# Performance work log

Hardware: AMD Instinct MI355X
Metric: run time of the kernel (lower is better)

Reference implementation:

```python
import jax, jax.numpy as jnp
import numpy as np

NUM_GROUPS = 32
EPS = 1e-6


def group_norm(x, w, b):
    # x: (B, C, L); normalize per group of C//32 channels over (channels-in-group, L)
    B, C, L = x.shape
    xg = x.reshape(B, NUM_GROUPS, C // NUM_GROUPS, L)
    mean = jnp.mean(xg, axis=(2, 3), keepdims=True)
    var = jnp.var(xg, axis=(2, 3), keepdims=True)
    xn = ((xg - mean) * jax.lax.rsqrt(var + EPS)).reshape(B, C, L)
    return xn * w[None, :, None] + b[None, :, None]


def conv1x1(x, w, b):
    # 1x1 Conv1d == channel-mixing linear. x: (B,C,L), w: (O,C), b: (O,)
    return jnp.einsum('oc,bcl->bol', w, x) + b[None, :, None]


def setup_inputs() -> dict:
    key = jax.random.key(0)
    ks = jax.random.split(key, 6)
    B, C, L = 8, 512, 2048
    s = 1.0 / np.sqrt(C)
    return {
        'x': jax.random.normal(ks[0], (B, C, L), dtype=jnp.float32),
        'gn_w': jnp.ones((C,), jnp.float32),
        'gn_b': jnp.zeros((C,), jnp.float32),
        'wq': jax.random.normal(ks[1], (C, C), dtype=jnp.float32) * s,
        'bq': jnp.zeros((C,), jnp.float32),
        'wk': jax.random.normal(ks[2], (C, C), dtype=jnp.float32) * s,
        'bk': jnp.zeros((C,), jnp.float32),
        'wv': jax.random.normal(ks[3], (C, C), dtype=jnp.float32) * s,
        'bv': jnp.zeros((C,), jnp.float32),
        'wo': jax.random.normal(ks[4], (C, C), dtype=jnp.float32) * s,
        'bo': jnp.zeros((C,), jnp.float32),
    }


def reference(x, gn_w, gn_b, wq, bq, wk, bk, wv, bv, wo, bo):
    B, C, L = x.shape
    h = group_norm(x, gn_w, gn_b)
    q = conv1x1(h, wq, bq)  # (B,C,L)
    k = conv1x1(h, wk, bk)
    v = conv1x1(h, wv, bv)
    scale = jnp.asarray(C, x.dtype) ** -0.5
    # scores over length: w[b,i,j] = sum_c q[b,c,i] k[b,c,j]
    w_ = jnp.einsum('bci,bcj->bij', q, k) * scale
    w_ = jax.nn.softmax(w_, axis=-1)
    # h[b,c,i] = sum_j w[b,i,j] v[b,c,j]
    h = jnp.einsum('bij,bcj->bci', w_, v)
    h = conv1x1(h, wo, bo)
    return x + h
```

## Files before the change

kernel.cpp:

```cpp
#include <hip/hip_runtime.h>
#include <math.h>

#define BATCH 8
#define CH 512
#define LEN 2048
#define NG 32
#define CPG 16

typedef unsigned short u16;
typedef __bf16 bf16x8 __attribute__((ext_vector_type(8)));
typedef float f32x16 __attribute__((ext_vector_type(16)));

__device__ __forceinline__ u16 f2bf(float f) {
    union { float f; unsigned u; } c; c.f = f;
    unsigned r = c.u + 0x7fffu + ((c.u >> 16) & 1u);
    return (u16)(r >> 16);
}
__device__ __forceinline__ float bf2f(u16 h) {
    union { unsigned u; float f; } c; c.u = ((unsigned)h) << 16;
    return c.f;
}
__device__ __forceinline__ void gload16(const u16* g, u16* l) {
    __builtin_amdgcn_global_load_lds(
        (const __attribute__((address_space(1))) unsigned int*)g,
        (__attribute__((address_space(3))) unsigned int*)l, 16, 0, 0);
}

__global__ __launch_bounds__(256) void fused_pre(
    const float* __restrict__ x,
    const float* __restrict__ w0, const float* __restrict__ w1,
    const float* __restrict__ w2, const float* __restrict__ w3,
    u16* __restrict__ o0, u16* __restrict__ o1,
    u16* __restrict__ o2, u16* __restrict__ o3,
    float4* __restrict__ zbuf, float* __restrict__ stats) {
    const int blk = blockIdx.x;
    if (blk < 16) {
        zbuf[blk * 256 + threadIdx.x] = make_float4(0.f, 0.f, 0.f, 0.f);
    } else if (blk < 1040) {
        const int wb = blk - 16;
        const float* s; u16* d;
        switch (wb >> 8) {
            case 0: s = w0; d = o0; break;
            case 1: s = w1; d = o1; break;
            case 2: s = w2; d = o2; break;
            default: s = w3; d = o3; break;
        }
        const int i = (wb & 255) * 256 + threadIdx.x;
        float4 f = ((const float4*)s)[i];
        ((ushort4*)d)[i] = make_ushort4(f2bf(f.x), f2bf(f.y), f2bf(f.z), f2bf(f.w));
    } else {
        const int sb = blk - 1040;
        const int b = sb >> 7, g = (sb >> 2) & 31, sl = sb & 3;
        const float4* xp = (const float4*)(x + ((size_t)b * CH + (size_t)g * CPG) * LEN) + sl * 2048;
        float s = 0.f, s2 = 0.f;
        #pragma unroll
        for (int i = 0; i < 8; ++i) {
            float4 v = xp[threadIdx.x + i * 256];
            s += v.x + v.y + v.z + v.w;
            s2 = fmaf(v.x, v.x, fmaf(v.y, v.y, fmaf(v.z, v.z, fmaf(v.w, v.w, s2))));
        }
        #pragma unroll
        for (int off = 32; off > 0; off >>= 1) {
            s  += __shfl_down(s, off, 64);
            s2 += __shfl_down(s2, off, 64);
        }
        __shared__ float sm[2][4];
        const int lane = threadIdx.x & 63, wv = threadIdx.x >> 6;
        if (lane == 0) { sm[0][wv] = s; sm[1][wv] = s2; }
        __syncthreads();
        if (threadIdx.x == 0) {
            const int base = (b * NG + g) * 4 + sl;
            stats[base]        = sm[0][0] + sm[0][1] + sm[0][2] + sm[0][3];
            stats[1024 + base] = sm[1][0] + sm[1][1] + sm[1][2] + sm[1][3];
        }
    }
}

__global__ __launch_bounds__(256) void gn_apply_t(const float* __restrict__ x,
                                                  const float* __restrict__ stats,
                                                  const float* __restrict__ gw,
                                                  const float* __restrict__ gb,
                                                  u16* __restrict__ Ht) {
    __shared__ float tile[64][65];
    const int b = blockIdx.z, c0 = blockIdx.y * 64, l0 = blockIdx.x * 64;
    const int t = threadIdx.x;
    const int rid = t >> 4, q = t & 15;
    const float inv = 1.f / (CPG * LEN);
    #pragma unroll
    for (int pass = 0; pass < 4; ++pass) {
        const int c = rid + pass * 16;
        const int ca = c0 + c;
        const int base = (b * NG + (ca >> 4)) * 4;
        const float S  = stats[base + 0] + stats[base + 1] + stats[base + 2] + stats[base + 3];
        const float S2 = stats[1024 + base + 0] + stats[1024 + base + 1]
                       + stats[1024 + base + 2] + stats[1024 + base + 3];
        const float mean = S * inv;
        const float var  = S2 * inv - mean * mean;
        const float a  = rsqrtf(var + 1e-6f) * gw[ca];
        const float sh = gb[ca] - mean * a;
        const float4 v = *(const float4*)&x[((size_t)b * CH + ca) * LEN + l0 + q * 4];
        tile[c][q * 4 + 0] = v.x * a + sh;
        tile[c][q * 4 + 1] = v.y * a + sh;
        tile[c][q * 4 + 2] = v.z * a + sh;
        tile[c][q * 4 + 3] = v.w * a + sh;
    }
    __syncthreads();
    #pragma unroll
    for (int pass = 0; pass < 4; ++pass) {
        const int l = rid + pass * 16;
        ushort4 o;
        o.x = f2bf(tile[q * 4 + 0][l]);
        o.y = f2bf(tile[q * 4 + 1][l]);
        o.z = f2bf(tile[q * 4 + 2][l]);
        o.w = f2bf(tile[q * 4 + 3][l]);
        *(ushort4*)&Ht[((size_t)b * LEN + l0 + l) * CH + c0 + q * 4] = o;
    }
}

#define EPI_QK   0
#define EPI_TNRM 3
#define EPI_FIN  4

template <int MODE>
__global__ __launch_bounds__(256, 4) void gemm_bt(
    const u16* __restrict__ A, int lda, long long sA,
    const u16* __restrict__ B, int ldb, long long sB,
    void* __restrict__ Out, void* __restrict__ Out2,
    int ldo, long long sO,
    const float* __restrict__ bias, const float* __restrict__ bias2,
    const float* __restrict__ res, long long sR,
    float* __restrict__ rsum, long long sRS,
    int K, float alpha) {
    __shared__ u16 As[128 * 64];
    __shared__ u16 Bs[128 * 64];

    int bz, by, bx;
    if (MODE == EPI_TNRM) {
        const int gx = gridDim.x, gy = gridDim.y;
        int flat = (blockIdx.z * gy + blockIdx.y) * gx + blockIdx.x;
        const int nbk = gx * gy * (int)gridDim.z;
        flat = (flat & 7) * (nbk >> 3) + (flat >> 3);
        bz = flat / (gx * gy);
        const int rr = flat - bz * gx * gy;
        by = rr & 3;
        bx = rr >> 2;
    } else {
        bz = blockIdx.z; by = blockIdx.y; bx = blockIdx.x;
    }
    const int n0 = bx * 128, m0 = by * 128;
    A += (size_t)bz * sA;
    B += (size_t)bz * sB;
    const int t = threadIdx.x;
    const int lane = t & 63, wid = t >> 6;

    const int rowL = t >> 3, kq = (t & 7) ^ (rowL & 7);
    unsigned aoff = (unsigned)((m0 + rowL) * lda + kq * 8);
    unsigned boff = (unsigned)((n0 + rowL) * ldb + kq * 8);
    u16* const lds_dst_a = As + t * 8;
    u16* const lds_dst_b = Bs + t * 8;

    f32x16 acc[2][2];
    #pragma unroll
    for (int i = 0; i < 2; ++i)
        #pragma unroll
        for (int j = 0; j < 2; ++j)
            acc[i][j] = (f32x16)(0.f);

    const int col = lane & 31, half = lane >> 5;
    const int wm = (wid & 1) * 64, wn = (wid >> 1) * 64;
    const int mf = wm + col, nf = wn + col;
    const int mswz = mf & 7, nswz = nf & 7;

    for (int k0 = 0; k0 < K; k0 += 64) {
        #pragma unroll
        for (int g = 0; g < 4; ++g) {
            gload16(A + aoff + g * (32 * lda), lds_dst_a + g * 2048);
            gload16(B + boff + g * (32 * ldb), lds_dst_b + g * 2048);
        }
        aoff += 64; boff += 64;
        __syncthreads();
        #pragma unroll
        for (int ks = 0; ks < 4; ++ks) {
            const int kcA = ((ks * 2 + half) ^ mswz) * 8;
            const int kcB = ((ks * 2 + half) ^ nswz) * 8;
            bf16x8 a0 = *(const bf16x8*)(As + (mf)      * 64 + kcA);
            bf16x8 a1 = *(const bf16x8*)(As + (mf + 32) * 64 + kcA);
            bf16x8 b0 = *(const bf16x8*)(Bs + (nf)      * 64 + kcB);
            bf16x8 b1 = *(const bf16x8*)(Bs + (nf + 32) * 64 + kcB);
            acc[0][0] = __builtin_amdgcn_mfma_f32_32x32x16_bf16(a0, b0, acc[0][0], 0, 0, 0);
            acc[0][1] = __builtin_amdgcn_mfma_f32_32x32x16_bf16(a0, b1, acc[0][1], 0, 0, 0);
            acc[1][0] = __builtin_amdgcn_mfma_f32_32x32x16_bf16(a1, b0, acc[1][0], 0, 0, 0);
            acc[1][1] = __builtin_amdgcn_mfma_f32_32x32x16_bf16(a1, b1, acc[1][1], 0, 0, 0);
        }
        __syncthreads();
    }

    if (MODE == EPI_FIN) {
        float* O = (float*)Out + (size_t)bz * sO;
        const float* R = res + (size_t)bz * sR;
        #pragma unroll
        for (int im = 0; im < 2; ++im)
            #pragma unroll
            for (int g4 = 0; g4 < 4; ++g4) {
                const int mb = m0 + wm + im * 32 + g4 * 8 + half * 4;
                #pragma unroll
                for (int jn = 0; jn < 2; ++jn) {
                    const int n = n0 + wn + jn * 32 + col;
                    const float bb = bias[n];
                    const size_t base = (size_t)n * ldo + mb;
                    const float4 r4 = *(const float4*)&R[base];
                    float4 o4;
                    o4.x = acc[im][jn][g4 * 4 + 0] + bb + r4.x;
                    o4.y = acc[im][jn][g4 * 4 + 1] + bb + r4.y;
                    o4.z = acc[im][jn][g4 * 4 + 2] + bb + r4.z;
                    o4.w = acc[im][jn][g4 * 4 + 3] + bb + r4.w;
                    *(float4*)&O[base] = o4;
                }
            }
    } else {
        u16* O;
        const float* bi = bias;
        const float* RS = (MODE == EPI_TNRM) ? rsum + (size_t)bz * sRS : nullptr;
        int mbase = m0 + wm;
        if (MODE == EPI_QK) {
            const bool hi = (m0 & 512) != 0;
            O  = (u16*)(hi ? Out2 : Out) + (size_t)bz * sO;
            bi = hi ? bias2 : bias;
            mbase = (m0 & 511) + wm;
        } else {
            O = (u16*)Out + (size_t)bz * sO;
        }
        float inv[2];
        if (MODE == EPI_TNRM) {
            inv[0] = 1.f / RS[n0 + wn + col];
            inv[1] = 1.f / RS[n0 + wn + 32 + col];
        }
        #pragma unroll
        for (int im = 0; im < 2; ++im)
            #pragma unroll
            for (int g4 = 0; g4 < 4; ++g4) {
                const int mb = mbase + im * 32 + g4 * 8 + half * 4;
                float4 bm = make_float4(0.f, 0.f, 0.f, 0.f);
                if (MODE == EPI_QK) bm = *(const float4*)&bi[mb];
                #pragma unroll
                for (int jn = 0; jn < 2; ++jn) {
                    const int n = n0 + wn + jn * 32 + col;
                    float v0 = acc[im][jn][g4 * 4 + 0];
                    float v1 = acc[im][jn][g4 * 4 + 1];
                    float v2 = acc[im][jn][g4 * 4 + 2];
                    float v3 = acc[im][jn][g4 * 4 + 3];
                    if (MODE == EPI_QK)  { v0 += bm.x; v1 += bm.y; v2 += bm.z; v3 += bm.w; }
                    if (MODE == EPI_TNRM) { v0 *= inv[jn]; v1 *= inv[jn]; v2 *= inv[jn]; v3 *= inv[jn]; }
                    ushort4 pk = make_ushort4(f2bf(v0), f2bf(v1), f2bf(v2), f2bf(v3));
                    *(ushort4*)&O[(size_t)n * ldo + mb] = pk;
                }
            }
    }
}

__global__ __launch_bounds__(256, 4) void gemm_sv(
    const u16* __restrict__ Kt, const u16* __restrict__ Qt,
    const u16* __restrict__ Ht, const u16* __restrict__ Wvb,
    u16* __restrict__ Sb, u16* __restrict__ Vb,
    const float* __restrict__ bv, float* __restrict__ rowsum,
    float alpha) {
    __shared__ u16 As[128 * 64];
    __shared__ u16 Bs[128 * 64];

    const long long sH = (long long)LEN * CH;
    const int blk = blockIdx.x;
    const bool isV = blk >= 2048;
    int bz, by, bx;
    const u16 *A, *B;
    u16* O;
    if (!isV) {
        int flat = (blk & 7) * 256 + (blk >> 3);
        bz = flat >> 8;
        const int rr = flat & 255;
        by = rr >> 4; bx = rr & 15;
        A = Kt + (size_t)bz * sH;
        B = Qt + (size_t)bz * sH;
        O = Sb + (size_t)bz * ((long long)LEN * LEN);
    } else {
        const int v = blk - 2048;
        bz = v >> 6;
        const int rr = v & 63;
        by = rr >> 2; bx = rr & 3;
        A = Ht + (size_t)bz * sH;
        B = Wvb;
        O = Vb + (size_t)bz * ((long long)CH * LEN);
    }

    const int n0 = bx * 128, m0 = by * 128;
    const int t = threadIdx.x;
    const int lane = t & 63, wid = t >> 6;

    const int rowL = t >> 3, kq = (t & 7) ^ (rowL & 7);
    unsigned aoff = (unsigned)((m0 + rowL) * CH + kq * 8);
    unsigned boff = (unsigned)((n0 + rowL) * CH + kq * 8);
    u16* const lds_dst_a = As + t * 8;
    u16* const lds_dst_b = Bs + t * 8;

    f32x16 acc[2][2];
    #pragma unroll
    for (int i = 0; i < 2; ++i)
        #pragma unroll
        for (int j = 0; j < 2; ++j)
            acc[i][j] = (f32x16)(0.f);

    const int col = lane & 31, half = lane >> 5;
    const int wm = (wid & 1) * 64, wn = (wid >> 1) * 64;
    const int mf = wm + col, nf = wn + col;
    const int mswz = mf & 7, nswz = nf & 7;

    for (int k0 = 0; k0 < CH; k0 += 64) {
        #pragma unroll
        for (int g = 0; g < 4; ++g) {
            gload16(A + aoff + g * (32 * CH), lds_dst_a + g * 2048);
            gload16(B + boff + g * (32 * CH), lds_dst_b + g * 2048);
        }
        aoff += 64; boff += 64;
        __syncthreads();
        #pragma unroll
        for (int ks = 0; ks < 4; ++ks) {
            const int kcA = ((ks * 2 + half) ^ mswz) * 8;
            const int kcB = ((ks * 2 + half) ^ nswz) * 8;
            bf16x8 a0 = *(const bf16x8*)(As + (mf)      * 64 + kcA);
            bf16x8 a1 = *(const bf16x8*)(As + (mf + 32) * 64 + kcA);
            bf16x8 b0 = *(const bf16x8*)(Bs + (nf)      * 64 + kcB);
            bf16x8 b1 = *(const bf16x8*)(Bs + (nf + 32) * 64 + kcB);
            acc[0][0] = __builtin_amdgcn_mfma_f32_32x32x16_bf16(a0, b0, acc[0][0], 0, 0, 0);
            acc[0][1] = __builtin_amdgcn_mfma_f32_32x32x16_bf16(a0, b1, acc[0][1], 0, 0, 0);
            acc[1][0] = __builtin_amdgcn_mfma_f32_32x32x16_bf16(a1, b0, acc[1][0], 0, 0, 0);
            acc[1][1] = __builtin_amdgcn_mfma_f32_32x32x16_bf16(a1, b1, acc[1][1], 0, 0, 0);
        }
        __syncthreads();
    }

    if (!isV) {
        float* RS = rowsum + (size_t)bz * LEN;
        float psum[2] = {0.f, 0.f};
        #pragma unroll
        for (int im = 0; im < 2; ++im)
            #pragma unroll
            for (int g4 = 0; g4 < 4; ++g4) {
                const int mb = m0 + wm + im * 32 + g4 * 8 + half * 4;
                #pragma unroll
                for (int jn = 0; jn < 2; ++jn) {
                    const int n = n0 + wn + jn * 32 + col;
                    u16 h0 = f2bf(__expf(acc[im][jn][g4 * 4 + 0] * alpha));
                    u16 h1 = f2bf(__expf(acc[im][jn][g4 * 4 + 1] * alpha));
                    u16 h2 = f2bf(__expf(acc[im][jn][g4 * 4 + 2] * alpha));
                    u16 h3 = f2bf(__expf(acc[im][jn][g4 * 4 + 3] * alpha));
                    psum[jn] += bf2f(h0) + bf2f(h1) + bf2f(h2) + bf2f(h3);
                    *(ushort4*)&O[(size_t)n * LEN + mb] = make_ushort4(h0, h1, h2, h3);
                }
            }
        #pragma unroll
        for (int jn = 0; jn < 2; ++jn) psum[jn] += __shfl_xor(psum[jn], 32, 64);
        if (half == 0) {
            #pragma unroll
            for (int jn = 0; jn < 2; ++jn)
                atomicAdd(&RS[n0 + wn + jn * 32 + col], psum[jn]);
        }
    } else {
        #pragma unroll
        for (int im = 0; im < 2; ++im)
            #pragma unroll
            for (int g4 = 0; g4 < 4; ++g4) {
                const int mb = m0 + wm + im * 32 + g4 * 8 + half * 4;
                #pragma unroll
                for (int jn = 0; jn < 2; ++jn) {
                    const int n = n0 + wn + jn * 32 + col;
                    const float bb = bv[n];
                    ushort4 pk = make_ushort4(f2bf(acc[im][jn][g4 * 4 + 0] + bb),
                                              f2bf(acc[im][jn][g4 * 4 + 1] + bb),
                                              f2bf(acc[im][jn][g4 * 4 + 2] + bb),
                                              f2bf(acc[im][jn][g4 * 4 + 3] + bb));
                    *(ushort4*)&O[(size_t)n * LEN + mb] = pk;
                }
            }
    }
}

extern "C" void kernel_launch(void* const* d_in, const int* in_sizes, int n_in,
                              void* d_out, int out_size, void* d_ws, size_t ws_size,
                              hipStream_t stream) {
    const float* x    = (const float*)d_in[0];
    const float* gn_w = (const float*)d_in[1];
    const float* gn_b = (const float*)d_in[2];
    const float* wq   = (const float*)d_in[3];
    const float* bq   = (const float*)d_in[4];
    const float* wk   = (const float*)d_in[5];
    const float* bk   = (const float*)d_in[6];
    const float* wv   = (const float*)d_in[7];
    const float* bv   = (const float*)d_in[8];
    const float* wo   = (const float*)d_in[9];
    const float* bo   = (const float*)d_in[10];
    float* out = (float*)d_out;

    char* p = (char*)d_ws;
    const size_t WSZ = (size_t)CH * CH * 2;
    const size_t HSZ = (size_t)BATCH * CH * LEN * 2;
    u16* Wqk = (u16*)p; p += 2 * WSZ;
    u16* Wvb = (u16*)p; p += WSZ;
    u16* Wob = (u16*)p; p += WSZ;
    u16* Ht  = (u16*)p; p += HSZ;
    u16* Qt  = (u16*)p; p += HSZ;
    u16* Kt  = (u16*)p; p += HSZ;
    u16* Vb  = (u16*)p; p += HSZ;
    u16* Sb  = (u16*)p; p += (size_t)BATCH * LEN * LEN * 2;
    float* rowsum = (float*)p; p += (size_t)BATCH * LEN * 4;
    float* stats  = (float*)p;

    const long long sH = (long long)LEN * CH;
    const long long sV = (long long)CH * LEN;
    const float scale = 0.04419417382415922f;

    fused_pre<<<2064, 256, 0, stream>>>(x, wq, wk, wv, wo,
                                        Wqk, Wqk + (size_t)CH * CH, Wvb, Wob,
                                        (float4*)rowsum, stats);
    gn_apply_t<<<dim3(LEN / 64, CH / 64, BATCH), 256, 0, stream>>>(x, stats, gn_w, gn_b, Ht);

    gemm_bt<EPI_QK><<<dim3(16, 8, 8), 256, 0, stream>>>(
        Wqk, CH, 0, Ht, CH, sH, Qt, Kt, CH, sH, bq, bk, nullptr, 0, nullptr, 0, CH, 0.f);
    gemm_sv<<<2560, 256, 0, stream>>>(Kt, Qt, Ht, Wvb, Sb, Vb, bv, rowsum, scale);
    gemm_bt<EPI_TNRM><<<dim3(16, 4, 8), 256, 0, stream>>>(
        Vb, LEN, sV, Sb, LEN, (long long)LEN * LEN, Ht, nullptr, CH, sH,
        nullptr, nullptr, nullptr, 0, rowsum, LEN, LEN, 0.f);
    gemm_bt<EPI_FIN><<<dim3(4, 16, 8), 256, 0, stream>>>(
        Ht, CH, sH, Wob, CH, 0, out, nullptr, LEN, sV, bo, nullptr, x, sV, nullptr, 0, CH, 0.f);
}
```

Baseline: 264.5 us.

## Fold output projection into value weights and fuse PV with final epilogue

Precomputes Wo·Wv in fp32 inside the prep kernel, along with a combined bias Wo·bv+bo, so the value GEMM produces Wo·V directly. The separate output-projection GEMM is removed. The P·V GEMM now writes the final fp32 output with rowsum normalization, bias and residual applied in its epilogue. This drops one 512-K GEMM and one bf16 intermediate round trip, at the cost of a slow scalar fp32 512x512x512 product in a 64-block prep section and different rounding.

```diff
diff --git a/kernel.cpp b/kernel.cpp
--- a/kernel.cpp
+++ b/kernel.cpp
@@ -28,34 +28,67 @@
 
 __global__ __launch_bounds__(256) void fused_pre(
     const float* __restrict__ x,
-    const float* __restrict__ w0, const float* __restrict__ w1,
-    const float* __restrict__ w2, const float* __restrict__ w3,
-    u16* __restrict__ o0, u16* __restrict__ o1,
-    u16* __restrict__ o2, u16* __restrict__ o3,
+    const float* __restrict__ wq, const float* __restrict__ wk,
+    const float* __restrict__ wv, const float* __restrict__ wo,
+    const float* __restrict__ bv, const float* __restrict__ bo,
+    u16* __restrict__ oq, u16* __restrict__ ok,
+    u16* __restrict__ wov, float* __restrict__ biasp,
     float4* __restrict__ zbuf, float* __restrict__ stats) {
     const int blk = blockIdx.x;
+    const int t = threadIdx.x;
     if (blk < 16) {
-        zbuf[blk * 256 + threadIdx.x] = make_float4(0.f, 0.f, 0.f, 0.f);
-    } else if (blk < 1040) {
+        zbuf[blk * 256 + t] = make_float4(0.f, 0.f, 0.f, 0.f);
+    } else if (blk < 528) {
         const int wb = blk - 16;
-        const float* s; u16* d;
-        switch (wb >> 8) {
-            case 0: s = w0; d = o0; break;
-            case 1: s = w1; d = o1; break;
-            case 2: s = w2; d = o2; break;
-            default: s = w3; d = o3; break;
-        }
-        const int i = (wb & 255) * 256 + threadIdx.x;
+        const float* s = (wb >> 8) ? wk : wq;
+        u16* d = (wb >> 8) ? ok : oq;
+        const int i = (wb & 255) * 256 + t;
         float4 f = ((const float4*)s)[i];
         ((ushort4*)d)[i] = make_ushort4(f2bf(f.x), f2bf(f.y), f2bf(f.z), f2bf(f.w));
+    } else if (blk < 592) {
+        const int b = blk - 528;
+        const int o0 = (b >> 3) * 64, c0 = (b & 7) * 64;
+        const int o = o0 + (t >> 4) * 4, c = c0 + (t & 15) * 4;
+        float acc[4][4] = {};
+        for (int k0 = 0; k0 < 512; k0 += 4) {
+            float4 A4[4], B4[4];
+            #pragma unroll
+            for (int r = 0; r < 4; ++r) A4[r] = *(const float4*)&wo[(size_t)(o + r) * 512 + k0];
+            #pragma unroll
+            for (int kk = 0; kk < 4; ++kk) B4[kk] = *(const float4*)&wv[(size_t)(k0 + kk) * 512 + c];
+            #pragma unroll
+            for (int r = 0; r < 4; ++r) {
+                const float ar[4] = {A4[r].x, A4[r].y, A4[r].z, A4[r].w};
+                #pragma unroll
+                for (int kk = 0; kk < 4; ++kk) {
+                    acc[r][0] = fmaf(ar[kk], B4[kk].x, acc[r][0]);
+                    acc[r][1] = fmaf(ar[kk], B4[kk].y, acc[r][1]);
+                    acc[r][2] = fmaf(ar[kk], B4[kk].z, acc[r][2]);
+                    acc[r][3] = fmaf(ar[kk], B4[kk].w, acc[r][3]);
+                }
+            }
+        }
+        #pragma unroll
+        for (int r = 0; r < 4; ++r)
+            *(ushort4*)&wov[(size_t)(o + r) * 512 + c] =
+                make_ushort4(f2bf(acc[r][0]), f2bf(acc[r][1]), f2bf(acc[r][2]), f2bf(acc[r][3]));
+    } else if (blk < 594) {
+        const int o = (blk - 592) * 256 + t;
+        float s = 0.f;
+        for (int kk = 0; kk < 512; kk += 4) {
+            float4 w4 = *(const float4*)&wo[(size_t)o * 512 + kk];
+            float4 b4 = *(const float4*)&bv[kk];
+            s = fmaf(w4.x, b4.x, fmaf(w4.y, b4.y, fmaf(w4.z, b4.z, fmaf(w4.w, b4.w, s))));
+        }
+        biasp[o] = s + bo[o];
     } else {
-        const int sb = blk - 1040;
+        const int sb = blk - 594;
         const int b = sb >> 7, g = (sb >> 2) & 31, sl = sb & 3;
         const float4* xp = (const float4*)(x + ((size_t)b * CH + (size_t)g * CPG) * LEN) + sl * 2048;
         float s = 0.f, s2 = 0.f;
         #pragma unroll
         for (int i = 0; i < 8; ++i) {
-            float4 v = xp[threadIdx.x + i * 256];
+            float4 v = xp[t + i * 256];
             s += v.x + v.y + v.z + v.w;
             s2 = fmaf(v.x, v.x, fmaf(v.y, v.y, fmaf(v.z, v.z, fmaf(v.w, v.w, s2))));
         }
@@ -65,10 +98,10 @@
             s2 += __shfl_down(s2, off, 64);
         }
         __shared__ float sm[2][4];
-        const int lane = threadIdx.x & 63, wv = threadIdx.x >> 6;
-        if (lane == 0) { sm[0][wv] = s; sm[1][wv] = s2; }
+        const int lane = t & 63, wvv = t >> 6;
+        if (lane == 0) { sm[0][wvv] = s; sm[1][wvv] = s2; }
         __syncthreads();
-        if (threadIdx.x == 0) {
+        if (t == 0) {
             const int base = (b * NG + g) * 4 + sl;
             stats[base]        = sm[0][0] + sm[0][1] + sm[0][2] + sm[0][3];
             stats[1024 + base] = sm[1][0] + sm[1][1] + sm[1][2] + sm[1][3];
@@ -118,8 +151,7 @@
 }
 
 #define EPI_QK   0
-#define EPI_TNRM 3
-#define EPI_FIN  4
+#define EPI_PVF  5
 
 template <int MODE>
 __global__ __launch_bounds__(256, 4) void gemm_bt(
@@ -135,15 +167,15 @@
     __shared__ u16 Bs[128 * 64];
 
     int bz, by, bx;
-    if (MODE == EPI_TNRM) {
+    if (MODE == EPI_PVF) {
         const int gx = gridDim.x, gy = gridDim.y;
         int flat = (blockIdx.z * gy + blockIdx.y) * gx + blockIdx.x;
         const int nbk = gx * gy * (int)gridDim.z;
         flat = (flat & 7) * (nbk >> 3) + (flat >> 3);
         bz = flat / (gx * gy);
         const int rr = flat - bz * gx * gy;
-        by = rr & 3;
-        bx = rr >> 2;
+        bx = rr & 3;
+        by = rr >> 2;
     } else {
         bz = blockIdx.z; by = blockIdx.y; bx = blockIdx.x;
     }
@@ -195,14 +227,17 @@
         __syncthreads();
     }
 
-    if (MODE == EPI_FIN) {
+    if (MODE == EPI_PVF) {
         float* O = (float*)Out + (size_t)bz * sO;
         const float* R = res + (size_t)bz * sR;
+        const float* RS = rsum + (size_t)bz * sRS;
         #pragma unroll
         for (int im = 0; im < 2; ++im)
             #pragma unroll
             for (int g4 = 0; g4 < 4; ++g4) {
                 const int mb = m0 + wm + im * 32 + g4 * 8 + half * 4;
+                const float4 rs4 = *(const float4*)&RS[mb];
+                const float4 iv = make_float4(1.f / rs4.x, 1.f / rs4.y, 1.f / rs4.z, 1.f / rs4.w);
                 #pragma unroll
                 for (int jn = 0; jn < 2; ++jn) {
                     const int n = n0 + wn + jn * 32 + col;
@@ -210,48 +245,31 @@
                     const size_t base = (size_t)n * ldo + mb;
                     const float4 r4 = *(const float4*)&R[base];
                     float4 o4;
-                    o4.x = acc[im][jn][g4 * 4 + 0] + bb + r4.x;
-                    o4.y = acc[im][jn][g4 * 4 + 1] + bb + r4.y;
-                    o4.z = acc[im][jn][g4 * 4 + 2] + bb + r4.z;
-                    o4.w = acc[im][jn][g4 * 4 + 3] + bb + r4.w;
+                    o4.x = acc[im][jn][g4 * 4 + 0] * iv.x + bb + r4.x;
+                    o4.y = acc[im][jn][g4 * 4 + 1] * iv.y + bb + r4.y;
+                    o4.z = acc[im][jn][g4 * 4 + 2] * iv.z + bb + r4.z;
+                    o4.w = acc[im][jn][g4 * 4 + 3] * iv.w + bb + r4.w;
                     *(float4*)&O[base] = o4;
                 }
             }
     } else {
-        u16* O;
-        const float* bi = bias;
-        const float* RS = (MODE == EPI_TNRM) ? rsum + (size_t)bz * sRS : nullptr;
-        int mbase = m0 + wm;
-        if (MODE == EPI_QK) {
-            const bool hi = (m0 & 512) != 0;
-            O  = (u16*)(hi ? Out2 : Out) + (size_t)bz * sO;
-            bi = hi ? bias2 : bias;
-            mbase = (m0 & 511) + wm;
-        } else {
-            O = (u16*)Out + (size_t)bz * sO;
-        }
-        float inv[2];
-        if (MODE == EPI_TNRM) {
-            inv[0] = 1.f / RS[n0 + wn + col];
-            inv[1] = 1.f / RS[n0 + wn + 32 + col];
-        }
+        const bool hi = (m0 & 512) != 0;
+        u16* O = (u16*)(hi ? Out2 : Out) + (size_t)bz * sO;
+        const float* bi = hi ? bias2 : bias;
+        const int mbase = (m0 & 511) + wm;
         #pragma unroll
         for (int im = 0; im < 2; ++im)
             #pragma unroll
             for (int g4 = 0; g4 < 4; ++g4) {
                 const int mb = mbase + im * 32 + g4 * 8 + half * 4;
-                float4 bm = make_float4(0.f, 0.f, 0.f, 0.f);
-                if (MODE == EPI_QK) bm = *(const float4*)&bi[mb];
+                const float4 bm = *(const float4*)&bi[mb];
                 #pragma unroll
                 for (int jn = 0; jn < 2; ++jn) {
                     const int n = n0 + wn + jn * 32 + col;
-                    float v0 = acc[im][jn][g4 * 4 + 0];
-                    float v1 = acc[im][jn][g4 * 4 + 1];
-                    float v2 = acc[im][jn][g4 * 4 + 2];
-                    float v3 = acc[im][jn][g4 * 4 + 3];
-                    if (MODE == EPI_QK)  { v0 += bm.x; v1 += bm.y; v2 += bm.z; v3 += bm.w; }
-                    if (MODE == EPI_TNRM) { v0 *= inv[jn]; v1 *= inv[jn]; v2 *= inv[jn]; v3 *= inv[jn]; }
-                    ushort4 pk = make_ushort4(f2bf(v0), f2bf(v1), f2bf(v2), f2bf(v3));
+                    ushort4 pk = make_ushort4(f2bf(acc[im][jn][g4 * 4 + 0] + bm.x),
+                                              f2bf(acc[im][jn][g4 * 4 + 1] + bm.y),
+                                              f2bf(acc[im][jn][g4 * 4 + 2] + bm.z),
+                                              f2bf(acc[im][jn][g4 * 4 + 3] + bm.w));
                     *(ushort4*)&O[(size_t)n * ldo + mb] = pk;
                 }
             }
@@ -260,10 +278,9 @@
 
 __global__ __launch_bounds__(256, 4) void gemm_sv(
     const u16* __restrict__ Kt, const u16* __restrict__ Qt,
-    const u16* __restrict__ Ht, const u16* __restrict__ Wvb,
+    const u16* __restrict__ Ht, const u16* __restrict__ Wov,
     u16* __restrict__ Sb, u16* __restrict__ Vb,
-    const float* __restrict__ bv, float* __restrict__ rowsum,
-    float alpha) {
+    float* __restrict__ rowsum, float alpha) {
     __shared__ u16 As[128 * 64];
     __shared__ u16 Bs[128 * 64];
 
@@ -287,7 +304,7 @@
         const int rr = v & 63;
         by = rr >> 2; bx = rr & 3;
         A = Ht + (size_t)bz * sH;
-        B = Wvb;
+        B = Wov;
         O = Vb + (size_t)bz * ((long long)CH * LEN);
     }
 
@@ -372,11 +389,10 @@
                 #pragma unroll
                 for (int jn = 0; jn < 2; ++jn) {
                     const int n = n0 + wn + jn * 32 + col;
-                    const float bb = bv[n];
-                    ushort4 pk = make_ushort4(f2bf(acc[im][jn][g4 * 4 + 0] + bb),
-                                              f2bf(acc[im][jn][g4 * 4 + 1] + bb),
-                                              f2bf(acc[im][jn][g4 * 4 + 2] + bb),
-                                              f2bf(acc[im][jn][g4 * 4 + 3] + bb));
+                    ushort4 pk = make_ushort4(f2bf(acc[im][jn][g4 * 4 + 0]),
+                                              f2bf(acc[im][jn][g4 * 4 + 1]),
+                                              f2bf(acc[im][jn][g4 * 4 + 2]),
+                                              f2bf(acc[im][jn][g4 * 4 + 3]));
                     *(ushort4*)&O[(size_t)n * LEN + mb] = pk;
                 }
             }
@@ -403,8 +419,8 @@
     const size_t WSZ = (size_t)CH * CH * 2;
     const size_t HSZ = (size_t)BATCH * CH * LEN * 2;
     u16* Wqk = (u16*)p; p += 2 * WSZ;
-    u16* Wvb = (u16*)p; p += WSZ;
-    u16* Wob = (u16*)p; p += WSZ;
+    u16* Wov = (u16*)p; p += WSZ;
+    float* biasp = (float*)p; p += WSZ;
     u16* Ht  = (u16*)p; p += HSZ;
     u16* Qt  = (u16*)p; p += HSZ;
     u16* Kt  = (u16*)p; p += HSZ;
@@ -417,17 +433,15 @@
     const long long sV = (long long)CH * LEN;
     const float scale = 0.04419417382415922f;
 
-    fused_pre<<<2064, 256, 0, stream>>>(x, wq, wk, wv, wo,
-                                        Wqk, Wqk + (size_t)CH * CH, Wvb, Wob,
+    fused_pre<<<1618, 256, 0, stream>>>(x, wq, wk, wv, wo, bv, bo,
+                                        Wqk, Wqk + (size_t)CH * CH, Wov, biasp,
                                         (float4*)rowsum, stats);
     gn_apply_t<<<dim3(LEN / 64, CH / 64, BATCH), 256, 0, stream>>>(x, stats, gn_w, gn_b, Ht);
 
     gemm_bt<EPI_QK><<<dim3(16, 8, 8), 256, 0, stream>>>(
         Wqk, CH, 0, Ht, CH, sH, Qt, Kt, CH, sH, bq, bk, nullptr, 0, nullptr, 0, CH, 0.f);
-    gemm_sv<<<2560, 256, 0, stream>>>(Kt, Qt, Ht, Wvb, Sb, Vb, bv, rowsum, scale);
-    gemm_bt<EPI_TNRM><<<dim3(16, 4, 8), 256, 0, stream>>>(
-        Vb, LEN, sV, Sb, LEN, (long long)LEN * LEN, Ht, nullptr, CH, sH,
-        nullptr, nullptr, nullptr, 0, rowsum, LEN, LEN, 0.f);
-    gemm_bt<EPI_FIN><<<dim3(4, 16, 8), 256, 0, stream>>>(
-        Ht, CH, sH, Wob, CH, 0, out, nullptr, LEN, sV, bo, nullptr, x, sV, nullptr, 0, CH, 0.f);
-}
+    gemm_sv<<<2560, 256, 0, stream>>>(Kt, Qt, Ht, Wov, Sb, Vb, rowsum, scale);
+    gemm_bt<EPI_PVF><<<dim3(4, 16, 8), 256, 0, stream>>>(
+        Sb, LEN, (long long)LEN * LEN, Vb, LEN, sV, out, nullptr, LEN, sV,
+        biasp, nullptr, x, sV, rowsum, LEN, LEN, 0.f);
+}
```

Result: slower. 288.1 us (+8.9%).
